# Kernel tuning notes

Measured on AMD Instinct MI355X. Metric: run time of the kernel, lower is better.

## Reference

```python
import jax, jax.numpy as jnp
import numpy as np

NEG_SLOPE = 0.2  # PyG GATConv default negative_slope


def _gat_dense(x, W, att_src, att_dst, bias):
    """PyG GATConv on a fully-connected graph (self-loops included) == dense attention.
    x: [N, F_in], W: [F_in, H*C], att_src/att_dst: [H, C], bias: [H*C] or [C].
    Returns per-head outputs [N, H, C] (bias added by caller after concat/mean).
    """
    H, C = att_src.shape
    N = x.shape[0]
    h = (x @ W).reshape(N, H, C)                      # transformed node feats
    s = jnp.einsum('nhc,hc->nh', h, att_src)          # alpha_src per source node
    t = jnp.einsum('nhc,hc->nh', h, att_dst)          # alpha_dst per dest node
    # e[i, j, h] = leaky_relu(alpha_dst[i] + alpha_src[j]); softmax over sources j
    e = jax.nn.leaky_relu(t[:, None, :] + s[None, :, :], NEG_SLOPE)  # [N, N, H]
    a = jax.nn.softmax(e, axis=1)
    out = jnp.einsum('ijh,jhc->ihc', a, h)            # aggregate sources -> dest
    return out


def setup_inputs() -> dict:
    key = jax.random.key(0)
    ks = jax.random.split(key, 11)
    N, D, C, H = 4096, 768, 128, 4
    sd1 = 1.0 / np.sqrt(D)
    sd2 = 1.0 / np.sqrt(H * C)
    sd3 = 1.0 / np.sqrt(C)
    return {
        'node_feats': jax.random.normal(ks[0], (N, D), dtype=jnp.float32),
        'W1': jax.random.normal(ks[1], (D, H * C), dtype=jnp.float32) * sd1,
        'att_src1': jax.random.normal(ks[2], (H, C), dtype=jnp.float32) * sd3,
        'att_dst1': jax.random.normal(ks[3], (H, C), dtype=jnp.float32) * sd3,
        'b1': jnp.zeros((H * C,), dtype=jnp.float32),
        'W2': jax.random.normal(ks[4], (H * C, C), dtype=jnp.float32) * sd2,
        'att_src2': jax.random.normal(ks[5], (1, C), dtype=jnp.float32) * sd3,
        'att_dst2': jax.random.normal(ks[6], (1, C), dtype=jnp.float32) * sd3,
        'b2': jnp.zeros((C,), dtype=jnp.float32),
        'fcW': jax.random.normal(ks[7], (C, D), dtype=jnp.float32) * sd3,
        'fcb': jnp.zeros((D,), dtype=jnp.float32),
    }


def reference(node_feats, W1, att_src1, att_dst1, b1, W2, att_src2, att_dst2, b2, fcW, fcb):
    N = node_feats.shape[0]
    # GAT layer 1: 4 heads, concat=True
    x = _gat_dense(node_feats, W1, att_src1, att_dst1, b1).reshape(N, -1) + b1
    x = jax.nn.elu(x)
    # GAT layer 2: 1 head, concat=False (mean over the single head == identity)
    x = _gat_dense(x, W2, att_src2, att_dst2, b2)[:, 0, :] + b2
    x = jax.nn.elu(x)
    x = x.mean(axis=0)            # [gat_hidden]
    return x @ fcW + fcb          # [hidden_dim]
```

## Files before the change

kernel.cpp:

```cpp
#include <hip/hip_runtime.h>
#include <hip/hip_bf16.h>


#define NNODE 4096
#define CDIM 128
#define TW 132
#define NEG 0.2f
#define CHUNK 64
#define NCHUNK 64
#define SEG 8
#define SEGK (NNODE / SEG)

typedef __bf16 bf16x8 __attribute__((ext_vector_type(8)));
typedef float f32x4 __attribute__((ext_vector_type(4)));

__device__ __forceinline__ unsigned short f2b(float f) {
  unsigned int u = __float_as_uint(f);
  u += 0x7fffu + ((u >> 16) & 1u);
  return (unsigned short)(u >> 16);
}

__global__ __launch_bounds__(256) void prep_kernel(const float* __restrict__ x,
                                                   const float* __restrict__ W1,
                                                   const float* __restrict__ W2,
                                                   unsigned short* __restrict__ xb,
                                                   unsigned short* __restrict__ W1t,
                                                   unsigned short* __restrict__ W2t) {
  __shared__ float tile[64][65];
  int b = blockIdx.x, t = threadIdx.x;
  if (b < 3072) {
    int i = b * 256 + t;
    float4 v = ((const float4*)x)[i];
    ushort4 o;
    o.x = f2b(v.x); o.y = f2b(v.y); o.z = f2b(v.z); o.w = f2b(v.w);
    ((ushort4*)xb)[i] = o;
    return;
  }
  const float* W; unsigned short* Wt; int K, N, n0, k0;
  if (b < 3072 + 96) {
    int b2 = b - 3072; W = W1; Wt = W1t; K = 768; N = 512;
    n0 = (b2 & 7) * 64; k0 = (b2 >> 3) * 64;
  } else {
    int b3 = b - 3072 - 96; W = W2; Wt = W2t; K = 512; N = 128;
    n0 = (b3 & 1) * 64; k0 = (b3 >> 1) * 64;
  }
  for (int p = 0; p < 16; p++) {
    int e = p * 256 + t;
    int rr = e >> 6, cc = e & 63;
    tile[rr][cc] = W[(size_t)(k0 + rr) * N + n0 + cc];
  }
  __syncthreads();
  for (int p = 0; p < 16; p++) {
    int e = p * 256 + t;
    int rr = e >> 6, cc = e & 63;
    Wt[(size_t)(n0 + rr) * K + k0 + cc] = f2b(tile[cc][rr]);
  }
}

template <int BM, int BN>
__global__ __launch_bounds__(256) void mfma_gemm_bt(const unsigned short* __restrict__ A,
                                                    const unsigned short* __restrict__ Bt,
                                                    float* __restrict__ C,
                                                    int M, int N, int K) {
  __shared__ __align__(16) unsigned short As[BM * 40];
  __shared__ __align__(16) unsigned short Bs[BN * 40];
  constexpr int WM = BM / 2, WN = BN / 2;
  constexpr int FI = WM / 16, FJ = WN / 16;
  constexpr int EA = BM * 32 / 8;
  constexpr int EB = BN * 32 / 8;
  constexpr int NA = (EA + 255) / 256;
  constexpr int NB = (EB + 255) / 256;
  int tid = threadIdx.x;
  int lane = tid & 63, wave = tid >> 6;
  int wm = (wave >> 1) * WM, wn = (wave & 1) * WN;
  int m0 = blockIdx.y * BM, n0 = blockIdx.x * BN;
  int fm = lane & 15, fq = lane >> 4;
  f32x4 acc[FI][FJ] = {};
  uint4 ar[NA], br[NB];
#pragma unroll
  for (int q = 0; q < NA; q++) {
    int e = q * 256 + tid;
    if (e < EA) {
      int r = e >> 2, kk = (e & 3) * 8;
      ar[q] = *(const uint4*)(A + (size_t)(m0 + r) * K + kk);
    }
  }
#pragma unroll
  for (int q = 0; q < NB; q++) {
    int e = q * 256 + tid;
    if (e < EB) {
      int r = e >> 2, kk = (e & 3) * 8;
      br[q] = *(const uint4*)(Bt + (size_t)(n0 + r) * K + kk);
    }
  }
  for (int k0 = 0; k0 < K; k0 += 32) {
    __syncthreads();
#pragma unroll
    for (int q = 0; q < NA; q++) {
      int e = q * 256 + tid;
      if (e < EA) {
        int r = e >> 2, kk = (e & 3) * 8;
        *(uint4*)&As[r * 40 + kk] = ar[q];
      }
    }
#pragma unroll
    for (int q = 0; q < NB; q++) {
      int e = q * 256 + tid;
      if (e < EB) {
        int r = e >> 2, kk = (e & 3) * 8;
        *(uint4*)&Bs[r * 40 + kk] = br[q];
      }
    }
    __syncthreads();
    if (k0 + 32 < K) {
#pragma unroll
      for (int q = 0; q < NA; q++) {
        int e = q * 256 + tid;
        if (e < EA) {
          int r = e >> 2, kk = (e & 3) * 8;
          ar[q] = *(const uint4*)(A + (size_t)(m0 + r) * K + k0 + 32 + kk);
        }
      }
#pragma unroll
      for (int q = 0; q < NB; q++) {
        int e = q * 256 + tid;
        if (e < EB) {
          int r = e >> 2, kk = (e & 3) * 8;
          br[q] = *(const uint4*)(Bt + (size_t)(n0 + r) * K + k0 + 32 + kk);
        }
      }
    }
    bf16x8 af[FI], bfr[FJ];
#pragma unroll
    for (int i = 0; i < FI; i++)
      af[i] = *(const bf16x8*)&As[(wm + i * 16 + fm) * 40 + fq * 8];
#pragma unroll
    for (int j = 0; j < FJ; j++)
      bfr[j] = *(const bf16x8*)&Bs[(wn + j * 16 + fm) * 40 + fq * 8];
#pragma unroll
    for (int i = 0; i < FI; i++)
#pragma unroll
      for (int j = 0; j < FJ; j++)
        acc[i][j] = __builtin_amdgcn_mfma_f32_16x16x32_bf16(af[i], bfr[j], acc[i][j], 0, 0, 0);
  }
#pragma unroll
  for (int i = 0; i < FI; i++) {
#pragma unroll
    for (int j = 0; j < FJ; j++) {
      int r = m0 + wm + i * 16 + fq * 4;
      int ccol = n0 + wn + j * 16 + fm;
#pragma unroll
      for (int reg = 0; reg < 4; reg++)
        C[(size_t)(r + reg) * N + ccol] = acc[i][j][reg];
    }
  }
}

__global__ void st_kernel(const float* __restrict__ h,
                          const float* __restrict__ asrc,
                          const float* __restrict__ adst,
                          float* __restrict__ s, float* __restrict__ t, int H) {
  int n = blockIdx.x;
  int wave = threadIdx.x >> 6, lane = threadIdx.x & 63;
  int HC = H * CDIM;
  float2 hv = *(const float2*)&h[(size_t)n * HC + wave * CDIM + lane * 2];
  float2 av = *(const float2*)&asrc[wave * CDIM + lane * 2];
  float2 dv = *(const float2*)&adst[wave * CDIM + lane * 2];
  float ps = hv.x * av.x + hv.y * av.y;
  float pt = hv.x * dv.x + hv.y * dv.y;
#pragma unroll
  for (int o = 32; o > 0; o >>= 1) {
    ps += __shfl_down(ps, o, 64);
    pt += __shfl_down(pt, o, 64);
  }
  if (lane == 0) {
    s[(size_t)wave * NNODE + n] = ps;
    t[(size_t)wave * NNODE + n] = pt;
  }
}

__global__ __launch_bounds__(256) void rank_count_kernel(const float* __restrict__ s,
                                                         int* __restrict__ partial) {
  __shared__ __align__(16) float keys[SEGK];
  int hh = blockIdx.z, seg = blockIdx.y, tid = threadIdx.x;
  const float* sp = s + (size_t)hh * NNODE;
  for (int k = tid; k < SEGK; k += 256) keys[k] = sp[seg * SEGK + k];
  __syncthreads();
  int mi = blockIdx.x * 256 + tid;
  float mk = sp[mi];
  int jbase = seg * SEGK;
  int cnt = 0;
#pragma unroll 4
  for (int j = 0; j < SEGK; j += 4) {
    float4 kv = *(const float4*)&keys[j];
    int jj = jbase + j;
    cnt += (kv.x < mk) || (kv.x == mk && (jj + 0) < mi);
    cnt += (kv.y < mk) || (kv.y == mk && (jj + 1) < mi);
    cnt += (kv.z < mk) || (kv.z == mk && (jj + 2) < mi);
    cnt += (kv.w < mk) || (kv.w == mk && (jj + 3) < mi);
  }
  partial[((size_t)hh * SEG + seg) * NNODE + mi] = cnt;
}

__global__ __launch_bounds__(256) void rank_scatter_kernel(const float* __restrict__ s,
                                                           const int* __restrict__ partial,
                                                           float* __restrict__ ss,
                                                           int* __restrict__ si) {
  int hh = blockIdx.y;
  int mi = blockIdx.x * 256 + threadIdx.x;
  int rank = 0;
#pragma unroll
  for (int g = 0; g < SEG; g++) rank += partial[((size_t)hh * SEG + g) * NNODE + mi];
  ss[(size_t)hh * NNODE + rank] = s[(size_t)hh * NNODE + mi];
  si[(size_t)hh * NNODE + rank] = mi;
}

__global__ __launch_bounds__(128) void passA_kernel(const float* __restrict__ h,
                                                    const float* __restrict__ ss,
                                                    const int* __restrict__ si,
                                                    float* __restrict__ partP,
                                                    float* __restrict__ partM, int H) {
  __shared__ float eP[CHUNK], eM[CHUNK];
  __shared__ int ids[CHUNK];
  int b = blockIdx.x, hh = b / NCHUNK, ci = b % NCHUNK;
  int c = threadIdx.x;
  int HC = H * CDIM;
  int base = ci * CHUNK;
  if (c < CHUNK) {
    float sv = ss[(size_t)hh * NNODE + base + c];
    ids[c] = si[(size_t)hh * NNODE + base + c];
    eP[c] = expf(sv);
    eM[c] = expf(NEG * sv);
  }
  __syncthreads();
  float sp = 0.f, sm = 0.f;
  for (int kb = 0; kb < CHUNK; kb += 8) {
    float v[8];
#pragma unroll
    for (int j = 0; j < 8; j++)
      v[j] = h[(size_t)ids[kb + j] * HC + hh * CDIM + c];
#pragma unroll
    for (int j = 0; j < 8; j++) {
      sp = fmaf(eP[kb + j], v[j], sp);
      sm = fmaf(eM[kb + j], v[j], sm);
    }
  }
  size_t o = ((size_t)hh * NCHUNK + ci) * TW;
  partP[o + c] = sp;
  partM[o + c] = sm;
  if (c == 0) {
    float zp = 0.f, zm = 0.f;
#pragma unroll
    for (int k = 0; k < CHUNK; k++) { zp += eP[k]; zm += eM[k]; }
    partP[o + 128] = zp;
    partM[o + 128] = zm;
  }
}

__global__ __launch_bounds__(128) void passC_kernel(const float* __restrict__ h,
                                                    const float* __restrict__ ss,
                                                    const int* __restrict__ si,
                                                    const float* __restrict__ partP,
                                                    const float* __restrict__ partM,
                                                    float* __restrict__ SS,
                                                    float* __restrict__ PP, int H) {
  __shared__ float hrow[CHUNK][CDIM];
  __shared__ float eP[CHUNK], eM[CHUNK];
  __shared__ int ids[CHUNK];
  int b = blockIdx.x, hh = b / NCHUNK, ci = b % NCHUNK;
  int c = threadIdx.x;
  int HC = H * CDIM;
  int base = ci * CHUNK;
  size_t hb = (size_t)hh * (NNODE + 1);
  if (c < CHUNK) {
    float sv = ss[(size_t)hh * NNODE + base + c];
    ids[c] = si[(size_t)hh * NNODE + base + c];
    eP[c] = expf(sv);
    eM[c] = expf(NEG * sv);
  }
  __syncthreads();
  float cm = 0.f, cp = 0.f;
  for (int g0 = 0; g0 < NCHUNK; g0 += 16) {
    float vm[16], vp[16];
#pragma unroll
    for (int j = 0; j < 16; j++) {
      size_t o = ((size_t)hh * NCHUNK + g0 + j) * TW + c;
      vm[j] = partM[o];
      vp[j] = partP[o];
    }
#pragma unroll
    for (int j = 0; j < 16; j++) {
      if (g0 + j < ci) cm += vm[j];
      if (g0 + j > ci) cp += vp[j];
    }
  }
  float zcm = 0.f, zcp = 0.f;
  if (c == 0) {
    for (int g0 = 0; g0 < NCHUNK; g0 += 16) {
      float vm[16], vp[16];
#pragma unroll
      for (int j = 0; j < 16; j++) {
        size_t o = ((size_t)hh * NCHUNK + g0 + j) * TW + 128;
        vm[j] = partM[o];
        vp[j] = partP[o];
      }
#pragma unroll
      for (int j = 0; j < 16; j++) {
        if (g0 + j < ci) zcm += vm[j];
        if (g0 + j > ci) zcp += vp[j];
      }
    }
  }
  for (int kb = 0; kb < CHUNK; kb += 8) {
    float v[8];
#pragma unroll
    for (int j = 0; j < 8; j++)
      v[j] = h[(size_t)ids[kb + j] * HC + hh * CDIM + c];
#pragma unroll
    for (int j = 0; j < 8; j++) hrow[kb + j][c] = v[j];
  }
  float runm = cm, runzm = zcm;
#pragma unroll 8
  for (int k = 0; k < CHUNK; k++) {
    size_t row = (hb + base + k) * TW;
    PP[row + c] = runm;
    if (c == 0) PP[row + 128] = runzm;
    runm = fmaf(eM[k], hrow[k][c], runm);
    runzm += eM[k];
  }
  if (ci == NCHUNK - 1) {
    size_t row = (hb + NNODE) * TW;
    PP[row + c] = runm;
    if (c == 0) PP[row + 128] = runzm;
  }
  float runp = cp, runzp = zcp;
#pragma unroll 8
  for (int k = CHUNK - 1; k >= 0; k--) {
    runp = fmaf(eP[k], hrow[k][c], runp);
    runzp += eP[k];
    size_t row = (hb + base + k) * TW;
    SS[row + c] = runp;
    if (c == 0) SS[row + 128] = runzp;
  }
  if (ci == NCHUNK - 1) {
    size_t row = (hb + NNODE) * TW;
    SS[row + c] = 0.f;
    if (c == 0) SS[row + 128] = 0.f;
  }
}

template <typename OUT>
__global__ __launch_bounds__(128) void attend_kernel(const float* __restrict__ SS,
                                                     const float* __restrict__ PP,
                                                     const float* __restrict__ ss,
                                                     const float* __restrict__ tt,
                                                     const float* __restrict__ bias,
                                                     OUT* __restrict__ out, int H) {
  int b = blockIdx.x;
  int n = b / H, hh = b % H;
  int c = threadIdx.x;
  float tv = tt[(size_t)hh * NNODE + n];
  const float* sp = ss + (size_t)hh * NNODE;
  float thr = -tv;
  int lo = 0, hi = NNODE;
  while (lo < hi) { int mid = (lo + hi) >> 1; if (sp[mid] < thr) lo = mid + 1; else hi = mid; }
  size_t hb = (size_t)hh * (NNODE + 1);
  float wp = expf(tv), wm = expf(NEG * tv);
  float num = wp * SS[(hb + lo) * TW + c] + wm * PP[(hb + lo) * TW + c];
  float Z = wp * SS[(hb + lo) * TW + 128] + wm * PP[(hb + lo) * TW + 128];
  float o = num / Z + bias[hh * CDIM + c];
  float r = (o > 0.f) ? o : (expf(o) - 1.f);
  if constexpr (sizeof(OUT) == 2)
    out[(size_t)n * (H * CDIM) + hh * CDIM + c] = f2b(r);
  else
    out[(size_t)n * (H * CDIM) + hh * CDIM + c] = r;
}

__global__ __launch_bounds__(256) void mean_kernel(const float* __restrict__ x,
                                                   float* __restrict__ m) {
  __shared__ float red[256];
  int c = blockIdx.x, tid = threadIdx.x;
  float acc = 0.f;
  for (int i = tid; i < NNODE; i += 256) acc += x[(size_t)i * CDIM + c];
  red[tid] = acc; __syncthreads();
  for (int o = 128; o > 0; o >>= 1) { if (tid < o) red[tid] += red[tid + o]; __syncthreads(); }
  if (tid == 0) m[c] = red[0] * (1.f / NNODE);
}

__global__ __launch_bounds__(256) void fc_kernel(const float* __restrict__ m,
                                                 const float* __restrict__ fcW,
                                                 const float* __restrict__ fcb,
                                                 float* __restrict__ out) {
  int d = blockIdx.x * 256 + threadIdx.x;
  float acc = fcb[d];
  for (int c2 = 0; c2 < CDIM; c2++) acc = fmaf(m[c2], fcW[c2 * 768 + d], acc);
  out[d] = acc;
}

extern "C" void kernel_launch(void* const* d_in, const int* in_sizes, int n_in,
                              void* d_out, int out_size, void* d_ws, size_t ws_size,
                              hipStream_t stream) {
  const float* x   = (const float*)d_in[0];
  const float* W1  = (const float*)d_in[1];
  const float* as1 = (const float*)d_in[2];
  const float* ad1 = (const float*)d_in[3];
  const float* b1  = (const float*)d_in[4];
  const float* W2  = (const float*)d_in[5];
  const float* as2 = (const float*)d_in[6];
  const float* ad2 = (const float*)d_in[7];
  const float* b2  = (const float*)d_in[8];
  const float* fcW = (const float*)d_in[9];
  const float* fcb = (const float*)d_in[10];

  float* ws = (float*)d_ws;
  size_t off = 0;
  auto alloc = [&](size_t nfloats) { float* p = ws + off; off += nfloats; return p; };

  float* h1  = alloc((size_t)NNODE * 512);
  float* x2f = alloc((size_t)NNODE * 256 + 64 + 16384);
  float* h2  = alloc((size_t)NNODE * 128);
  float* x3  = alloc((size_t)NNODE * 128);
  float* s1  = alloc((size_t)4 * NNODE);
  float* t1  = alloc((size_t)4 * NNODE);
  float* sS1 = alloc((size_t)4 * NNODE);
  int*   sI1 = (int*)alloc((size_t)4 * NNODE);
  float* SS1 = alloc((size_t)4 * (NNODE + 1) * TW);
  float* PP1 = alloc((size_t)4 * (NNODE + 1) * TW);
  float* pP1 = alloc((size_t)4 * NCHUNK * TW);
  float* pM1 = alloc((size_t)4 * NCHUNK * TW);
  float* s2  = alloc(NNODE);
  float* t2  = alloc(NNODE);
  float* sS2 = alloc(NNODE);
  int*   sI2 = (int*)alloc(NNODE);
  float* SS2 = alloc((size_t)(NNODE + 1) * TW);
  float* PP2 = alloc((size_t)(NNODE + 1) * TW);
  float* pP2 = alloc((size_t)NCHUNK * TW);
  float* pM2 = alloc((size_t)NCHUNK * TW);
  float* mv  = alloc(128);
  int*   rparts = (int*)alloc((size_t)4 * SEG * NNODE);

  unsigned short* xb  = (unsigned short*)PP1;
  unsigned short* W1t = (unsigned short*)SS1;
  unsigned short* x2b = (unsigned short*)x2f;
  unsigned short* W2t = (unsigned short*)(x2f + NNODE * 256 + 64);

  prep_kernel<<<3072 + 96 + 16, 256, 0, stream>>>(x, W1, W2, xb, W1t, W2t);
  mfma_gemm_bt<64, 64><<<dim3(512 / 64, NNODE / 64), 256, 0, stream>>>(xb, W1t, h1, NNODE, 512, 768);
  st_kernel<<<NNODE, 4 * 64, 0, stream>>>(h1, as1, ad1, s1, t1, 4);
  rank_count_kernel<<<dim3(NNODE / 256, SEG, 4), 256, 0, stream>>>(s1, rparts);
  rank_scatter_kernel<<<dim3(NNODE / 256, 4), 256, 0, stream>>>(s1, rparts, sS1, sI1);
  passA_kernel<<<4 * NCHUNK, 128, 0, stream>>>(h1, sS1, sI1, pP1, pM1, 4);
  passC_kernel<<<4 * NCHUNK, 128, 0, stream>>>(h1, sS1, sI1, pP1, pM1, SS1, PP1, 4);
  attend_kernel<unsigned short><<<NNODE * 4, 128, 0, stream>>>(SS1, PP1, sS1, t1, b1, x2b, 4);
  mfma_gemm_bt<32, 64><<<dim3(128 / 64, NNODE / 32), 256, 0, stream>>>(x2b, W2t, h2, NNODE, 128, 512);
  st_kernel<<<NNODE, 1 * 64, 0, stream>>>(h2, as2, ad2, s2, t2, 1);
  rank_count_kernel<<<dim3(NNODE / 256, SEG, 1), 256, 0, stream>>>(s2, rparts);
  rank_scatter_kernel<<<dim3(NNODE / 256, 1), 256, 0, stream>>>(s2, rparts, sS2, sI2);
  passA_kernel<<<NCHUNK, 128, 0, stream>>>(h2, sS2, sI2, pP2, pM2, 1);
  passC_kernel<<<NCHUNK, 128, 0, stream>>>(h2, sS2, sI2, pP2, pM2, SS2, PP2, 1);
  attend_kernel<float><<<NNODE, 128, 0, stream>>>(SS2, PP2, sS2, t2, b2, x3, 1);
  mean_kernel<<<128, 256, 0, stream>>>(x3, mv);
  fc_kernel<<<3, 256, 0, stream>>>(mv, fcW, fcb, (float*)d_out);
}
```

Baseline: 227.1 us.

## Fuse attention-score projection into GEMM epilogue and merge rank and mean/fc kernels

Computes the per-node source and destination attention scores inside the MFMA GEMM epilogue with wave shuffles and atomicAdd. This removes the separate st_kernel and a re-read of h. The rank count and scatter kernels are merged into one block-level rank sort that splits the counting across 8 thread groups. Mean and fc are fused using a last-block counter, and the accumulators are zeroed inside prep_kernel. This reduces launch count and intermediate traffic, at the cost of float atomics whose summation order is nondeterministic.

After: 245.5 us. 8.1% more time.

```diff
diff --git a/kernel.cpp b/kernel.cpp
--- a/kernel.cpp
+++ b/kernel.cpp
@@ -8,8 +8,6 @@
 #define NEG 0.2f
 #define CHUNK 64
 #define NCHUNK 64
-#define SEG 8
-#define SEGK (NNODE / SEG)
 
 typedef __bf16 bf16x8 __attribute__((ext_vector_type(8)));
 typedef float f32x4 __attribute__((ext_vector_type(4)));
@@ -25,7 +23,10 @@
                                                    const float* __restrict__ W2,
                                                    unsigned short* __restrict__ xb,
                                                    unsigned short* __restrict__ W1t,
-                                                   unsigned short* __restrict__ W2t) {
+                                                   unsigned short* __restrict__ W2t,
+                                                   float* __restrict__ zs1,
+                                                   float* __restrict__ zs2,
+                                                   float* __restrict__ zfc) {
   __shared__ float tile[64][65];
   int b = blockIdx.x, t = threadIdx.x;
   if (b < 3072) {
@@ -36,6 +37,17 @@
     ((ushort4*)xb)[i] = o;
     return;
   }
+  if (b >= 3184) {
+    float4 z = {0.f, 0.f, 0.f, 0.f};
+    if (b < 3216) {
+      ((float4*)zs1)[(b - 3184) * 256 + t] = z;
+    } else if (b < 3224) {
+      ((float4*)zs2)[(b - 3216) * 256 + t] = z;
+    } else if (t < 64) {
+      ((float4*)zfc)[t] = z;
+    }
+    return;
+  }
   const float* W; unsigned short* Wt; int K, N, n0, k0;
   if (b < 3072 + 96) {
     int b2 = b - 3072; W = W1; Wt = W1t; K = 768; N = 512;
@@ -61,7 +73,11 @@
 __global__ __launch_bounds__(256) void mfma_gemm_bt(const unsigned short* __restrict__ A,
                                                     const unsigned short* __restrict__ Bt,
                                                     float* __restrict__ C,
-                                                    int M, int N, int K) {
+                                                    int M, int N, int K,
+                                                    float* __restrict__ sAcc,
+                                                    float* __restrict__ tAcc,
+                                                    const float* __restrict__ av_s,
+                                                    const float* __restrict__ av_d) {
   __shared__ __align__(16) unsigned short As[BM * 40];
   __shared__ __align__(16) unsigned short Bs[BN * 40];
   constexpr int WM = BM / 2, WN = BN / 2;
@@ -154,65 +170,73 @@
         C[(size_t)(r + reg) * N + ccol] = acc[i][j][reg];
     }
   }
-}
-
-__global__ void st_kernel(const float* __restrict__ h,
-                          const float* __restrict__ asrc,
-                          const float* __restrict__ adst,
-                          float* __restrict__ s, float* __restrict__ t, int H) {
-  int n = blockIdx.x;
-  int wave = threadIdx.x >> 6, lane = threadIdx.x & 63;
-  int HC = H * CDIM;
-  float2 hv = *(const float2*)&h[(size_t)n * HC + wave * CDIM + lane * 2];
-  float2 av = *(const float2*)&asrc[wave * CDIM + lane * 2];
-  float2 dv = *(const float2*)&adst[wave * CDIM + lane * 2];
-  float ps = hv.x * av.x + hv.y * av.y;
-  float pt = hv.x * dv.x + hv.y * dv.y;
-#pragma unroll
-  for (int o = 32; o > 0; o >>= 1) {
-    ps += __shfl_down(ps, o, 64);
-    pt += __shfl_down(pt, o, 64);
-  }
-  if (lane == 0) {
-    s[(size_t)wave * NNODE + n] = ps;
-    t[(size_t)wave * NNODE + n] = pt;
-  }
-}
-
-__global__ __launch_bounds__(256) void rank_count_kernel(const float* __restrict__ s,
-                                                         int* __restrict__ partial) {
-  __shared__ __align__(16) float keys[SEGK];
-  int hh = blockIdx.z, seg = blockIdx.y, tid = threadIdx.x;
+  {
+    int hh = n0 >> 7;
+    float avs[FJ], avd[FJ];
+#pragma unroll
+    for (int j = 0; j < FJ; j++) {
+      int col = n0 + wn + j * 16 + fm;
+      avs[j] = av_s[col];
+      avd[j] = av_d[col];
+    }
+#pragma unroll
+    for (int i = 0; i < FI; i++) {
+#pragma unroll
+      for (int reg = 0; reg < 4; reg++) {
+        float sv = 0.f, tv = 0.f;
+#pragma unroll
+        for (int j = 0; j < FJ; j++) {
+          sv = fmaf(acc[i][j][reg], avs[j], sv);
+          tv = fmaf(acc[i][j][reg], avd[j], tv);
+        }
+#pragma unroll
+        for (int o = 1; o < 16; o <<= 1) {
+          sv += __shfl_xor(sv, o, 64);
+          tv += __shfl_xor(tv, o, 64);
+        }
+        if (fm == 0) {
+          int row = m0 + wm + i * 16 + fq * 4 + reg;
+          atomicAdd(&sAcc[(size_t)hh * NNODE + row], sv);
+          atomicAdd(&tAcc[(size_t)hh * NNODE + row], tv);
+        }
+      }
+    }
+  }
+}
+
+__global__ __launch_bounds__(256) void rank_sort_kernel(const float* __restrict__ s,
+                                                        float* __restrict__ ss,
+                                                        int* __restrict__ si) {
+  __shared__ __align__(16) float keys[NNODE];
+  __shared__ int pc[8][32];
+  int hh = blockIdx.y, tid = threadIdx.x;
   const float* sp = s + (size_t)hh * NNODE;
-  for (int k = tid; k < SEGK; k += 256) keys[k] = sp[seg * SEGK + k];
-  __syncthreads();
-  int mi = blockIdx.x * 256 + tid;
-  float mk = sp[mi];
-  int jbase = seg * SEGK;
+  for (int k = tid; k < NNODE / 4; k += 256)
+    ((float4*)keys)[k] = ((const float4*)sp)[k];
+  __syncthreads();
+  int slot = tid & 31, part = tid >> 5;
+  int node = blockIdx.x * 32 + slot;
+  float mk = keys[node];
   int cnt = 0;
+  int j0 = part * 512;
 #pragma unroll 4
-  for (int j = 0; j < SEGK; j += 4) {
+  for (int j = j0; j < j0 + 512; j += 4) {
     float4 kv = *(const float4*)&keys[j];
-    int jj = jbase + j;
-    cnt += (kv.x < mk) || (kv.x == mk && (jj + 0) < mi);
-    cnt += (kv.y < mk) || (kv.y == mk && (jj + 1) < mi);
-    cnt += (kv.z < mk) || (kv.z == mk && (jj + 2) < mi);
-    cnt += (kv.w < mk) || (kv.w == mk && (jj + 3) < mi);
-  }
-  partial[((size_t)hh * SEG + seg) * NNODE + mi] = cnt;
-}
-
-__global__ __launch_bounds__(256) void rank_scatter_kernel(const float* __restrict__ s,
-                                                           const int* __restrict__ partial,
-                                                           float* __restrict__ ss,
-                                                           int* __restrict__ si) {
-  int hh = blockIdx.y;
-  int mi = blockIdx.x * 256 + threadIdx.x;
-  int rank = 0;
-#pragma unroll
-  for (int g = 0; g < SEG; g++) rank += partial[((size_t)hh * SEG + g) * NNODE + mi];
-  ss[(size_t)hh * NNODE + rank] = s[(size_t)hh * NNODE + mi];
-  si[(size_t)hh * NNODE + rank] = mi;
+    cnt += (kv.x < mk) || (kv.x == mk && (j + 0) < node);
+    cnt += (kv.y < mk) || (kv.y == mk && (j + 1) < node);
+    cnt += (kv.z < mk) || (kv.z == mk && (j + 2) < node);
+    cnt += (kv.w < mk) || (kv.w == mk && (j + 3) < node);
+  }
+  pc[part][slot] = cnt;
+  __syncthreads();
+  if (tid < 32) {
+    int rank = 0;
+#pragma unroll
+    for (int p = 0; p < 8; p++) rank += pc[p][tid];
+    int n2 = blockIdx.x * 32 + tid;
+    ss[(size_t)hh * NNODE + rank] = keys[n2];
+    si[(size_t)hh * NNODE + rank] = n2;
+  }
 }
 
 __global__ __launch_bounds__(128) void passA_kernel(const float* __restrict__ h,
@@ -376,25 +400,40 @@
     out[(size_t)n * (H * CDIM) + hh * CDIM + c] = r;
 }
 
-__global__ __launch_bounds__(256) void mean_kernel(const float* __restrict__ x,
-                                                   float* __restrict__ m) {
+__global__ __launch_bounds__(256) void mean_fc_kernel(const float* __restrict__ x,
+                                                      const float* __restrict__ fcW,
+                                                      const float* __restrict__ fcb,
+                                                      float* __restrict__ mv,
+                                                      int* __restrict__ counter,
+                                                      float* __restrict__ out) {
   __shared__ float red[256];
+  __shared__ float m[CDIM];
+  __shared__ int lastFlag;
   int c = blockIdx.x, tid = threadIdx.x;
   float acc = 0.f;
   for (int i = tid; i < NNODE; i += 256) acc += x[(size_t)i * CDIM + c];
   red[tid] = acc; __syncthreads();
   for (int o = 128; o > 0; o >>= 1) { if (tid < o) red[tid] += red[tid + o]; __syncthreads(); }
-  if (tid == 0) m[c] = red[0] * (1.f / NNODE);
-}
-
-__global__ __launch_bounds__(256) void fc_kernel(const float* __restrict__ m,
-                                                 const float* __restrict__ fcW,
-                                                 const float* __restrict__ fcb,
-                                                 float* __restrict__ out) {
-  int d = blockIdx.x * 256 + threadIdx.x;
-  float acc = fcb[d];
-  for (int c2 = 0; c2 < CDIM; c2++) acc = fmaf(m[c2], fcW[c2 * 768 + d], acc);
-  out[d] = acc;
+  if (tid == 0) {
+    __hip_atomic_store(&mv[c], red[0] * (1.f / NNODE), __ATOMIC_RELEASE,
+                       __HIP_MEMORY_SCOPE_AGENT);
+    int old = __hip_atomic_fetch_add(counter, 1, __ATOMIC_ACQ_REL,
+                                     __HIP_MEMORY_SCOPE_AGENT);
+    lastFlag = (old == 127);
+  }
+  __syncthreads();
+  if (!lastFlag) return;
+  if (tid < CDIM)
+    m[tid] = __hip_atomic_load(&mv[tid], __ATOMIC_ACQUIRE, __HIP_MEMORY_SCOPE_AGENT);
+  __syncthreads();
+#pragma unroll
+  for (int d0 = 0; d0 < 3; d0++) {
+    int d = d0 * 256 + tid;
+    float a = fcb[d];
+#pragma unroll 4
+    for (int c2 = 0; c2 < CDIM; c2++) a = fmaf(m[c2], fcW[c2 * 768 + d], a);
+    out[d] = a;
+  }
 }
 
 extern "C" void kernel_launch(void* const* d_in, const int* in_sizes, int n_in,
@@ -436,29 +475,28 @@
   float* PP2 = alloc((size_t)(NNODE + 1) * TW);
   float* pP2 = alloc((size_t)NCHUNK * TW);
   float* pM2 = alloc((size_t)NCHUNK * TW);
-  float* mv  = alloc(128);
-  int*   rparts = (int*)alloc((size_t)4 * SEG * NNODE);
+  float* fcaux = alloc(256);
+
+  float* mv = fcaux;
+  int* counter = (int*)(fcaux + 128);
 
   unsigned short* xb  = (unsigned short*)PP1;
   unsigned short* W1t = (unsigned short*)SS1;
   unsigned short* x2b = (unsigned short*)x2f;
   unsigned short* W2t = (unsigned short*)(x2f + NNODE * 256 + 64);
 
-  prep_kernel<<<3072 + 96 + 16, 256, 0, stream>>>(x, W1, W2, xb, W1t, W2t);
-  mfma_gemm_bt<64, 64><<<dim3(512 / 64, NNODE / 64), 256, 0, stream>>>(xb, W1t, h1, NNODE, 512, 768);
-  st_kernel<<<NNODE, 4 * 64, 0, stream>>>(h1, as1, ad1, s1, t1, 4);
-  rank_count_kernel<<<dim3(NNODE / 256, SEG, 4), 256, 0, stream>>>(s1, rparts);
-  rank_scatter_kernel<<<dim3(NNODE / 256, 4), 256, 0, stream>>>(s1, rparts, sS1, sI1);
+  prep_kernel<<<3225, 256, 0, stream>>>(x, W1, W2, xb, W1t, W2t, s1, s2, fcaux);
+  mfma_gemm_bt<64, 64><<<dim3(512 / 64, NNODE / 64), 256, 0, stream>>>(
+      xb, W1t, h1, NNODE, 512, 768, s1, t1, as1, ad1);
+  rank_sort_kernel<<<dim3(NNODE / 32, 4), 256, 0, stream>>>(s1, sS1, sI1);
   passA_kernel<<<4 * NCHUNK, 128, 0, stream>>>(h1, sS1, sI1, pP1, pM1, 4);
   passC_kernel<<<4 * NCHUNK, 128, 0, stream>>>(h1, sS1, sI1, pP1, pM1, SS1, PP1, 4);
   attend_kernel<unsigned short><<<NNODE * 4, 128, 0, stream>>>(SS1, PP1, sS1, t1, b1, x2b, 4);
-  mfma_gemm_bt<32, 64><<<dim3(128 / 64, NNODE / 32), 256, 0, stream>>>(x2b, W2t, h2, NNODE, 128, 512);
-  st_kernel<<<NNODE, 1 * 64, 0, stream>>>(h2, as2, ad2, s2, t2, 1);
-  rank_count_kernel<<<dim3(NNODE / 256, SEG, 1), 256, 0, stream>>>(s2, rparts);
-  rank_scatter_kernel<<<dim3(NNODE / 256, 1), 256, 0, stream>>>(s2, rparts, sS2, sI2);
+  mfma_gemm_bt<32, 64><<<dim3(128 / 64, NNODE / 32), 256, 0, stream>>>(
+      x2b, W2t, h2, NNODE, 128, 512, s2, t2, as2, ad2);
+  rank_sort_kernel<<<dim3(NNODE / 32, 1), 256, 0, stream>>>(s2, sS2, sI2);
   passA_kernel<<<NCHUNK, 128, 0, stream>>>(h2, sS2, sI2, pP2, pM2, 1);
   passC_kernel<<<NCHUNK, 128, 0, stream>>>(h2, sS2, sI2, pP2, pM2, SS2, PP2, 1);
   attend_kernel<float><<<NNODE, 128, 0, stream>>>(SS2, PP2, sS2, t2, b2, x3, 1);
-  mean_kernel<<<128, 256, 0, stream>>>(x3, mv);
-  fc_kernel<<<3, 256, 0, stream>>>(mv, fcW, fcb, (float*)d_out);
-}
+  mean_fc_kernel<<<128, 256, 0, stream>>>(x3, fcW, fcb, mv, counter, (float*)d_out);
+}
```
